# Kernel optimization log

Hardware: AMD Instinct MI355X
Metric: run time of the kernel (lower is better)

Reference implementation:

```python
import jax, jax.numpy as jnp
import numpy as np
from jax import lax

N, T, H, E = 50000, 200, 128, 1600000


def setup_inputs() -> dict:
    key = jax.random.key(0)
    ks = jax.random.split(key, 32)
    s = 0.05
    inp = {}
    inp["lightcurve"] = jax.random.normal(ks[0], (N, T), dtype=jnp.float32)
    inp["edge_index"] = jax.random.randint(ks[1], (2, E), 0, N, dtype=jnp.int32)
    # LSTM layer 0 (input_dim=1) and layer 1 (input H), PyTorch gate order i,f,g,o
    inp["W_ih0"] = jax.random.normal(ks[2], (4 * H, 1), jnp.float32) * s
    inp["W_hh0"] = jax.random.normal(ks[3], (4 * H, H), jnp.float32) * s
    inp["b_ih0"] = jnp.zeros((4 * H,), jnp.float32)
    inp["b_hh0"] = jnp.zeros((4 * H,), jnp.float32)
    inp["W_ih1"] = jax.random.normal(ks[4], (4 * H, H), jnp.float32) * s
    inp["W_hh1"] = jax.random.normal(ks[5], (4 * H, H), jnp.float32) * s
    inp["b_ih1"] = jnp.zeros((4 * H,), jnp.float32)
    inp["b_hh1"] = jnp.zeros((4 * H,), jnp.float32)
    # 3 GCN conv layers + LayerNorms
    for i in range(3):
        inp[f"Wg{i}"] = jax.random.normal(ks[6 + i], (H, H), jnp.float32) * s
        inp[f"bg{i}"] = jnp.zeros((H,), jnp.float32)
        inp[f"gamma{i}"] = jnp.ones((H,), jnp.float32)
        inp[f"beta{i}"] = jnp.zeros((H,), jnp.float32)
    inp["W_out"] = jax.random.normal(ks[10], (H, 1), jnp.float32) * s
    inp["b_out"] = jnp.zeros((1,), jnp.float32)
    return inp


def _lstm_encode(x, W_ih0, W_hh0, b_ih0, b_hh0, W_ih1, W_hh1, b_ih1, b_hh1):
    # x: [N, T, 1] -> final hidden of layer 2: [N, H]. Both layers fused in one scan.
    n = x.shape[0]
    h = W_hh0.shape[1]

    def cell(xt, hs, cs, Wih, Whh, bih, bhh):
        g = xt @ Wih.T + hs @ Whh.T + (bih + bhh)
        i, f, gg, o = jnp.split(g, 4, axis=-1)
        cs = jax.nn.sigmoid(f) * cs + jax.nn.sigmoid(i) * jnp.tanh(gg)
        hs = jax.nn.sigmoid(o) * jnp.tanh(cs)
        return hs, cs

    def step(carry, x_t):
        h1, c1, h2, c2 = carry
        h1, c1 = cell(x_t, h1, c1, W_ih0, W_hh0, b_ih0, b_hh0)
        h2, c2 = cell(h1, h2, c2, W_ih1, W_hh1, b_ih1, b_hh1)
        return (h1, c1, h2, c2), None

    z = jnp.zeros((n, h), x.dtype)
    (_, _, h2, _), _ = lax.scan(step, (z, z, z, z), jnp.swapaxes(x, 0, 1))
    return h2


def _forward(lightcurve, W_ih0, W_hh0, b_ih0, b_hh0, W_ih1, W_hh1, b_ih1, b_hh1,
             Wg0, bg0, gamma0, beta0, Wg1, bg1, gamma1, beta1, Wg2, bg2, gamma2, beta2,
             W_out, b_out, edge_index):
    n = lightcurve.shape[0]
    h = _lstm_encode(lightcurve[..., None], W_ih0, W_hh0, b_ih0, b_hh0,
                     W_ih1, W_hh1, b_ih1, b_hh1)
    # GCN normalization (PyG GCNConv defaults: add self-loops, symmetric norm)
    loops = jnp.arange(n, dtype=edge_index.dtype)
    row = jnp.concatenate([edge_index[0], loops])  # source
    col = jnp.concatenate([edge_index[1], loops])  # target
    deg = jax.ops.segment_sum(jnp.ones_like(col, dtype=h.dtype), col, num_segments=n)
    dinv = lax.rsqrt(jnp.maximum(deg, 1.0))
    enorm = dinv[row] * dinv[col]  # [E+N]
    for Wg, bg, gm, bt in ((Wg0, bg0, gamma0, beta0), (Wg1, bg1, gamma1, beta1), (Wg2, bg2, gamma2, beta2)):
        h_prev = h
        msg = (h @ Wg)[row] * enorm[:, None]            # gather + scale
        h = jax.ops.segment_sum(msg, col, num_segments=n) + bg  # scatter-add
        mu = h.mean(-1, keepdims=True)                  # LayerNorm
        var = jnp.mean((h - mu) ** 2, axis=-1, keepdims=True)
        h = (h - mu) * lax.rsqrt(var + 1e-5) * gm + bt
        h = jax.nn.relu(h)
        h = h + h_prev  # dropout is identity in eval mode
    pooled = h.mean(axis=0, keepdims=True)  # [1, H]
    return pooled @ W_out + b_out           # [1, 1]


def reference(lightcurve, edge_index, W_ih0, W_hh0, b_ih0, b_hh0,
              W_ih1, W_hh1, b_ih1, b_hh1,
              Wg0, bg0, gamma0, beta0, Wg1, bg1, gamma1, beta1,
              Wg2, bg2, gamma2, beta2, W_out, b_out):
    return _forward(lightcurve, W_ih0, W_hh0, b_ih0, b_hh0, W_ih1, W_hh1, b_ih1, b_hh1,
                    Wg0, bg0, gamma0, beta0, Wg1, bg1, gamma1, beta1,
                    Wg2, bg2, gamma2, beta2, W_out, b_out, edge_index)
```

## Files before the change

kernel.cpp:

```cpp
#include <hip/hip_runtime.h>

#define NN 50000
#define TT 200
#define HH 128
#define EE 1600000

typedef _Float16 f16x8 __attribute__((ext_vector_type(8)));
typedef float f32x4 __attribute__((ext_vector_type(4)));

__device__ __forceinline__ float sigf(float x) {
    return __builtin_amdgcn_rcpf(1.f + __expf(-x));
}
__device__ __forceinline__ float tanhf_(float x) {
    return 1.f - 2.f * __builtin_amdgcn_rcpf(__expf(2.f * x) + 1.f);
}
__device__ __forceinline__ f32x4 sig4(f32x4 x) {
    f32x4 r; r[0] = sigf(x[0]); r[1] = sigf(x[1]); r[2] = sigf(x[2]); r[3] = sigf(x[3]); return r;
}
__device__ __forceinline__ f32x4 tanh4(f32x4 x) {
    f32x4 r; r[0] = tanhf_(x[0]); r[1] = tanhf_(x[1]); r[2] = tanhf_(x[2]); r[3] = tanhf_(x[3]); return r;
}
__device__ __forceinline__ f32x4 splat4(float s) { f32x4 r = {s, s, s, s}; return r; }
__device__ __forceinline__ unsigned short f2h_bits(float x) {
    _Float16 h = (_Float16)x;
    union { _Float16 h; unsigned short u; } cv; cv.h = h; return cv.u;
}
__device__ __forceinline__ float h2f_bits(unsigned short u) {
    union { _Float16 h; unsigned short u; } cv; cv.u = u; return (float)cv.h;
}

__global__ void pack_w(const float* __restrict__ W, unsigned short* __restrict__ out) {
    int tile = blockIdx.x;
    int jn = tile >> 2, kk = tile & 3;
    int L = threadIdx.x;
    int n = jn * 16 + (L & 15);
    int k0 = kk * 32 + (L >> 4) * 8;
    unsigned short* dst = out + (size_t)tile * 512 + L * 8;
#pragma unroll
    for (int i = 0; i < 8; ++i) dst[i] = f2h_bits(W[n * 128 + k0 + i]);
}

__global__ void bias_prep(const float* __restrict__ bih0, const float* __restrict__ bhh0,
                          const float* __restrict__ bih1, const float* __restrict__ bhh1,
                          const float* __restrict__ wih0,
                          float* __restrict__ b0g, float* __restrict__ b1g, float* __restrict__ wxg) {
    int i = blockIdx.x * 256 + threadIdx.x;
    if (i < 512) {
        b0g[i] = bih0[i] + bhh0[i];
        b1g[i] = bih1[i] + bhh1[i];
        wxg[i] = wih0[i];
    }
}

__global__ void transpose_lc(const float* __restrict__ lc, float* __restrict__ xT) {
    __shared__ float tile[32][33];
    int tx = threadIdx.x, ty = threadIdx.y;
    int n0 = blockIdx.y * 32, t0 = blockIdx.x * 32;
#pragma unroll
    for (int i = 0; i < 32; i += 8) {
        int n = n0 + ty + i, t = t0 + tx;
        if (n < NN && t < TT) tile[ty + i][tx] = lc[(size_t)n * TT + t];
    }
    __syncthreads();
#pragma unroll
    for (int i = 0; i < 32; i += 8) {
        int t = t0 + ty + i, n = n0 + tx;
        if (n < NN && t < TT) xT[(size_t)t * NN + n] = tile[tx][ty + i];
    }
}


#define MFMA16(A, B, C) __builtin_amdgcn_mfma_f32_16x16x32_f16((A), (B), (C), 0, 0, 0)

#define MMC(HB, PI, PF, PG, PO, KK) {                                          \
    f16x8 bI_ = *reinterpret_cast<const f16x8*>((PI) + (KK) * 512);            \
    f16x8 bF_ = *reinterpret_cast<const f16x8*>((PF) + (KK) * 512);            \
    f16x8 bG_ = *reinterpret_cast<const f16x8*>((PG) + (KK) * 512);            \
    f16x8 bO_ = *reinterpret_cast<const f16x8*>((PO) + (KK) * 512);            \
    f16x8 a0_ = *reinterpret_cast<const f16x8*>(&(HB)[col][(KK) * 32 + quad * 8]);      \
    f16x8 a1_ = *reinterpret_cast<const f16x8*>(&(HB)[16 + col][(KK) * 32 + quad * 8]); \
    aI0 = MFMA16(a0_, bI_, aI0); aI1 = MFMA16(a1_, bI_, aI1);                  \
    aF0 = MFMA16(a0_, bF_, aF0); aF1 = MFMA16(a1_, bF_, aF1);                  \
    aG0 = MFMA16(a0_, bG_, aG0); aG1 = MFMA16(a1_, bG_, aG1);                  \
    aO0 = MFMA16(a0_, bO_, aO0); aO1 = MFMA16(a1_, bO_, aO1);                  \
}

#define ACT0N(RT, C, H, AI, AF, AG, AO) {                                      \
    f32x4 xv_ = *reinterpret_cast<const f32x4*>(&xs[(RT) * 16 + quad * 4]);    \
    f32x4 gi_ = AI + splat4(bI) + xv_ * splat4(wI);                            \
    f32x4 gf_ = AF + splat4(bF) + xv_ * splat4(wF);                            \
    f32x4 gg_ = AG + splat4(bG) + xv_ * splat4(wG);                            \
    f32x4 go_ = AO + splat4(bO) + xv_ * splat4(wO);                            \
    C = sig4(gf_) * C + sig4(gi_) * tanh4(gg_);                                \
    H = sig4(go_) * tanh4(C);                                                  \
}

#define ACT1N(C, H, AI, AF, AG, AO) {                                          \
    f32x4 gi_ = AI + splat4(bI);                                               \
    f32x4 gf_ = AF + splat4(bF);                                               \
    f32x4 gg_ = AG + splat4(bG);                                               \
    f32x4 go_ = AO + splat4(bO);                                               \
    C = sig4(gf_) * C + sig4(gi_) * tanh4(gg_);                                \
    H = sig4(go_) * tanh4(C);                                                  \
}

#define WRH(HB, RT, H)                                                         \
    (HB)[(RT) * 16 + quad * 4 + 0][j_] = f2h_bits((H)[0]);                     \
    (HB)[(RT) * 16 + quad * 4 + 1][j_] = f2h_bits((H)[1]);                     \
    (HB)[(RT) * 16 + quad * 4 + 2][j_] = f2h_bits((H)[2]);                     \
    (HB)[(RT) * 16 + quad * 4 + 3][j_] = f2h_bits((H)[3]);

#define STEP(PB, RB, T)                                                        \
    {                      \
        f32x4 aI0 = {}, aI1 = {}, aF0 = {}, aF1 = {};                          \
        f32x4 aG0 = {}, aG1 = {}, aO0 = {}, aO1 = {};                          \
        MMC(h1s[RB], p0I, p0F, p0G, p0O, 0)                                    \
        MMC(h1s[RB], p0I, p0F, p0G, p0O, 1)                                    \
        MMC(h1s[RB], p0I, p0F, p0G, p0O, 2)                                    \
        MMC(h1s[RB], p0I, p0F, p0G, p0O, 3)                                    \
        const float bI = b0s[j_], bF = b0s[128 + j_];                          \
        const float bG = b0s[256 + j_], bO = b0s[384 + j_];                    \
        const float wI = wxs[j_], wF = wxs[128 + j_];                          \
        const float wG = wxs[256 + j_], wO = wxs[384 + j_];                    \
        f32x4 h1v0, h1v1;                                                      \
        ACT0N(0, c1_0, h1v0, aI0, aF0, aG0, aO0)                               \
        ACT0N(1, c1_1, h1v1, aI1, aF1, aG1, aO1)                               \
        WRH(h1s[PB], 0, h1v0)                                                  \
        WRH(h1s[PB], 1, h1v1)                                                  \
    }                                                                          \
    __syncthreads();                                                           \
    {             \
        f32x4 aI0 = {}, aI1 = {}, aF0 = {}, aF1 = {};                          \
        f32x4 aG0 = {}, aG1 = {}, aO0 = {}, aO1 = {};                          \
        MMC(h1s[PB], u0I, u0F, u0G, u0O, 0)                                    \
        MMC(h1s[PB], u0I, u0F, u0G, u0O, 1)                                    \
        MMC(h1s[PB], u0I, u0F, u0G, u0O, 2)                                    \
        MMC(h1s[PB], u0I, u0F, u0G, u0O, 3)                                    \
        MMC(h2s[RB], v0I, v0F, v0G, v0O, 0)                                    \
        MMC(h2s[RB], v0I, v0F, v0G, v0O, 1)                                    \
        MMC(h2s[RB], v0I, v0F, v0G, v0O, 2)                                    \
        MMC(h2s[RB], v0I, v0F, v0G, v0O, 3)                                    \
        const float bI = b1s[j_], bF = b1s[128 + j_];                          \
        const float bG = b1s[256 + j_], bO = b1s[384 + j_];                    \
        f32x4 h2v0, h2v1;                                                      \
        ACT1N(c2_0, h2v0, aI0, aF0, aG0, aO0)                                  \
        ACT1N(c2_1, h2v1, aI1, aF1, aG1, aO1)                                  \
        WRH(h2s[PB], 0, h2v0)                                                  \
        WRH(h2s[PB], 1, h2v1)                                                  \
        if (tid < 32) {                                                        \
            int n_ = n0 + tid;                                                 \
            xs[tid] = ((T) + 1 < TT && n_ < NN)                                \
                          ? xT[(size_t)((T) + 1) * NN + n_] : 0.f;             \
        }                                                                      \
    }                                                                          \
    __syncthreads();

__global__ __launch_bounds__(512, 2) void lstm_kernel(
    const float* __restrict__ xT,
    const unsigned short* __restrict__ w0p,
    const unsigned short* __restrict__ w1ip,
    const unsigned short* __restrict__ w1hp,
    const float* __restrict__ b0g, const float* __restrict__ b1g,
    const float* __restrict__ wxg,
    float* __restrict__ h2out) {
    __shared__ unsigned short h1s[2][32][136];
    __shared__ unsigned short h2s[2][32][136];
    __shared__ __align__(16) float xs[32];
    __shared__ float b0s[512], b1s[512], wxs[512];

    const int tid = threadIdx.x;
    const int w = tid >> 6;
    const int lane = tid & 63;
    const int col = lane & 15;
    const int quad = lane >> 4;
    const int n0 = blockIdx.x * 32;
    const int j_ = w * 16 + col;

    for (int i = tid; i < 2 * 32 * 136; i += 512) {
        (&h1s[0][0][0])[i] = 0; (&h2s[0][0][0])[i] = 0;
    }
    if (tid < 512) { b0s[tid] = b0g[tid]; b1s[tid] = b1g[tid]; wxs[tid] = wxg[tid]; }
    if (tid < 32) { int n = n0 + tid; xs[tid] = (n < NN) ? xT[n] : 0.f; }

    const unsigned short* p0I = w0p + (size_t)w * 2048 + lane * 8;
    const unsigned short* p0F = w0p + (size_t)(8 + w) * 2048 + lane * 8;
    const unsigned short* p0G = w0p + (size_t)(16 + w) * 2048 + lane * 8;
    const unsigned short* p0O = w0p + (size_t)(24 + w) * 2048 + lane * 8;
    const unsigned short* u0I = w1ip + (size_t)w * 2048 + lane * 8;
    const unsigned short* u0F = w1ip + (size_t)(8 + w) * 2048 + lane * 8;
    const unsigned short* u0G = w1ip + (size_t)(16 + w) * 2048 + lane * 8;
    const unsigned short* u0O = w1ip + (size_t)(24 + w) * 2048 + lane * 8;
    const unsigned short* v0I = w1hp + (size_t)w * 2048 + lane * 8;
    const unsigned short* v0F = w1hp + (size_t)(8 + w) * 2048 + lane * 8;
    const unsigned short* v0G = w1hp + (size_t)(16 + w) * 2048 + lane * 8;
    const unsigned short* v0O = w1hp + (size_t)(24 + w) * 2048 + lane * 8;

    f32x4 c1_0 = {}, c1_1 = {}, c2_0 = {}, c2_1 = {};

    __syncthreads();

#pragma unroll 1
    for (int tt = 0; tt < TT; tt += 2) {
        STEP(0, 1, tt)
        STEP(1, 0, tt + 1)
    }

    for (int i = tid; i < 32 * 128; i += 512) {
        int m = i >> 7, j = i & 127;
        int n = n0 + m;
        if (n < NN) h2out[(size_t)n * HH + j] = h2f_bits(h2s[1][m][j]);
    }
}

__global__ void deg_init(float* __restrict__ deg) {
    int i = blockIdx.x * 256 + threadIdx.x;
    if (i < NN) deg[i] = 1.f;
}
__global__ void deg_edges(const int* __restrict__ ei, float* __restrict__ deg) {
    int e = blockIdx.x * 256 + threadIdx.x;
    if (e < EE) unsafeAtomicAdd(&deg[ei[EE + e]], 1.f);
}
__global__ void dinv_k(const float* __restrict__ deg, float* __restrict__ dinv) {
    int i = blockIdx.x * 256 + threadIdx.x;
    if (i < NN) dinv[i] = rsqrtf(fmaxf(deg[i], 1.f));
}

__global__ void scan_off(const float* __restrict__ deg, int* __restrict__ off) {
    __shared__ int sp[256];
    const int tid = threadIdx.x;
    const int chunk = (NN + 255) / 256;
    const int i0 = tid * chunk;
    int s = 0;
    for (int i = 0; i < chunk; ++i) {
        int idx = i0 + i;
        if (idx < NN) s += (int)deg[idx] - 1;
    }
    sp[tid] = s;
    __syncthreads();
    for (int o = 1; o < 256; o <<= 1) {
        int v = (tid >= o) ? sp[tid - o] : 0;
        __syncthreads();
        sp[tid] += v;
        __syncthreads();
    }
    int run = sp[tid] - s;
    for (int i = 0; i < chunk; ++i) {
        int idx = i0 + i;
        if (idx < NN) { off[idx] = run; run += (int)deg[idx] - 1; }
    }
    if (tid == 255) off[NN] = sp[255];
}

__global__ void csr_fill(const int* __restrict__ ei, const float* __restrict__ dinv,
                         const int* __restrict__ off, int* __restrict__ cur,
                         int* __restrict__ crow, float* __restrict__ cw) {
    int e = blockIdx.x * 256 + threadIdx.x;
    if (e >= EE) return;
    int r = ei[e], c = ei[EE + e];
    int p = atomicAdd(&cur[c], 1);
    int idx = off[c] + p;
    crow[idx] = r;
    cw[idx] = dinv[r] * dinv[c];
}

__global__ void gcn_gemm(const float* __restrict__ h, const float* __restrict__ Wg,
                         float* __restrict__ hw) {
    __shared__ float hsT[128][36];
    int tid = threadIdx.x;
    int n0 = blockIdx.x * 32;
#pragma unroll
    for (int c = 0; c < 16; ++c) {
        int lin = c * 256 + tid;
        int m = lin >> 7, k = lin & 127;
        int n = n0 + m;
        hsT[k][m] = (n < NN) ? h[(size_t)n * HH + k] : 0.f;
    }
    __syncthreads();
    int j = tid & 127, p = tid >> 7;
    float acc[16];
#pragma unroll
    for (int m = 0; m < 16; ++m) acc[m] = 0.f;
    for (int k = 0; k < 128; ++k) {
        float wg = Wg[k * 128 + j];
        const float4* hp = reinterpret_cast<const float4*>(&hsT[k][p * 16]);
        float4 a = hp[0], b = hp[1], c = hp[2], d = hp[3];
        acc[0]  += a.x * wg; acc[1]  += a.y * wg; acc[2]  += a.z * wg; acc[3]  += a.w * wg;
        acc[4]  += b.x * wg; acc[5]  += b.y * wg; acc[6]  += b.z * wg; acc[7]  += b.w * wg;
        acc[8]  += c.x * wg; acc[9]  += c.y * wg; acc[10] += c.z * wg; acc[11] += c.w * wg;
        acc[12] += d.x * wg; acc[13] += d.y * wg; acc[14] += d.z * wg; acc[15] += d.w * wg;
    }
#pragma unroll
    for (int m = 0; m < 16; ++m) {
        int n = n0 + p * 16 + m;
        if (n < NN) hw[(size_t)n * HH + j] = acc[m];
    }
}

__global__ __launch_bounds__(256) void gcn_agg(
    const float* __restrict__ hw, const int* __restrict__ off,
    const int* __restrict__ crow, const float* __restrict__ cw,
    const float* __restrict__ dinv, const float* __restrict__ bg,
    const float* __restrict__ gamma, const float* __restrict__ beta,
    float* __restrict__ h) {
    __shared__ float xch[4][2];
    const int tid = threadIdx.x;
    const int half = tid >> 7;
    const int f = tid & 127;
    const int v = blockIdx.x * 2 + half;
    const float d = dinv[v];
    float acc = bg[f] + d * d * hw[v * HH + f];
    const int s1 = off[v + 1];
    for (int s = off[v]; s < s1; ++s) {
        int r = crow[s];
        float wv = cw[s];
        acc = fmaf(wv, hw[r * HH + f], acc);
    }
    float sum = acc, sq = acc * acc;
#pragma unroll
    for (int o = 32; o; o >>= 1) { sum += __shfl_xor(sum, o); sq += __shfl_xor(sq, o); }
    int wid = tid >> 6;
    if ((tid & 63) == 0) { xch[wid][0] = sum; xch[wid][1] = sq; }
    __syncthreads();
    sum += xch[wid ^ 1][0]; sq += xch[wid ^ 1][1];
    float mu = sum * (1.f / 128.f);
    float var = sq * (1.f / 128.f) - mu * mu;
    float rn = rsqrtf(var + 1e-5f);
    float o = (acc - mu) * rn * gamma[f] + beta[f];
    h[v * HH + f] = fmaxf(o, 0.f) + h[v * HH + f];
}

__global__ void pool_k(const float* __restrict__ h, float* __restrict__ pooled) {
    int j = threadIdx.x & 127, p = threadIdx.x >> 7;
    float s = 0.f;
    for (int n = blockIdx.x * 2 + p; n < NN; n += 512) s += h[(size_t)n * HH + j];
    unsafeAtomicAdd(&pooled[j], s);
}

__global__ void final_k(const float* __restrict__ pooled, const float* __restrict__ Wout,
                        const float* __restrict__ bout, float* __restrict__ out) {
    int lane = threadIdx.x;
    float s = pooled[lane] * Wout[lane] + pooled[lane + 64] * Wout[lane + 64];
#pragma unroll
    for (int o = 32; o; o >>= 1) s += __shfl_xor(s, o);
    if (lane == 0) out[0] = s * (1.f / (float)NN) + bout[0];
}

extern "C" void kernel_launch(void* const* d_in, const int* in_sizes, int n_in,
                              void* d_out, int out_size, void* d_ws, size_t ws_size,
                              hipStream_t stream) {
    const float* lc   = (const float*)d_in[0];
    const int*   ei   = (const int*)d_in[1];
    const float* Wih0 = (const float*)d_in[2];
    const float* Whh0 = (const float*)d_in[3];
    const float* bih0 = (const float*)d_in[4];
    const float* bhh0 = (const float*)d_in[5];
    const float* Wih1 = (const float*)d_in[6];
    const float* Whh1 = (const float*)d_in[7];
    const float* bih1 = (const float*)d_in[8];
    const float* bhh1 = (const float*)d_in[9];
    const float* Wout = (const float*)d_in[22];
    const float* bout = (const float*)d_in[23];
    float* out = (float*)d_out;

    float* ws   = (float*)d_ws;
    float* h    = ws;
    float* hw   = ws + 6400000;
    float* xT   = ws + 6400000;
    int*   off  = (int*)(ws + 12800000);
    int*   cur  = off + 50048;
    int*   crow = cur + 50048;
    float* cw   = (float*)(crow + EE);
    float* P      = ws + 16400064;
    float* deg    = P;
    float* dinv   = deg + 50000;
    float* b0g    = dinv + 50000;
    float* b1g    = b0g + 512;
    float* wxg    = b1g + 512;
    float* pooled = wxg + 512;
    unsigned short* w0p  = (unsigned short*)(pooled + 128);
    unsigned short* w1ip = w0p + 65536;
    unsigned short* w1hp = w1ip + 65536;

    pack_w<<<128, 64, 0, stream>>>(Whh0, w0p);
    pack_w<<<128, 64, 0, stream>>>(Wih1, w1ip);
    pack_w<<<128, 64, 0, stream>>>(Whh1, w1hp);
    bias_prep<<<2, 256, 0, stream>>>(bih0, bhh0, bih1, bhh1, Wih0, b0g, b1g, wxg);
    {
        dim3 g((TT + 31) / 32, (NN + 31) / 32), b(32, 8);
        transpose_lc<<<g, b, 0, stream>>>(lc, xT);
    }
    deg_init<<<(NN + 255) / 256, 256, 0, stream>>>(deg);
    deg_edges<<<(EE + 255) / 256, 256, 0, stream>>>(ei, deg);
    dinv_k<<<(NN + 255) / 256, 256, 0, stream>>>(deg, dinv);

    lstm_kernel<<<(NN + 31) / 32, 512, 0, stream>>>(xT, w0p, w1ip, w1hp, b0g, b1g, wxg, h);

    hipMemsetAsync(cur, 0, 50000 * sizeof(int), stream);
    scan_off<<<1, 256, 0, stream>>>(deg, off);
    csr_fill<<<(EE + 255) / 256, 256, 0, stream>>>(ei, dinv, off, cur, crow, cw);

    for (int l = 0; l < 3; ++l) {
        const float* Wg = (const float*)d_in[10 + 4 * l];
        const float* bg = (const float*)d_in[11 + 4 * l];
        const float* gm = (const float*)d_in[12 + 4 * l];
        const float* bt = (const float*)d_in[13 + 4 * l];
        gcn_gemm<<<(NN + 31) / 32, 256, 0, stream>>>(h, Wg, hw);
        gcn_agg<<<NN / 2, 256, 0, stream>>>(hw, off, crow, cw, dinv, bg, gm, bt, h);
    }

    hipMemsetAsync(pooled, 0, HH * sizeof(float), stream);
    pool_k<<<256, 256, 0, stream>>>(h, pooled);
    final_k<<<1, 64, 0, stream>>>(pooled, Wout, bout, out);
}
```

Baseline: 7.872 ms.

## Skew LSTM layers across timesteps to use one barrier per step

```diff
diff --git a/kernel.cpp b/kernel.cpp
--- a/kernel.cpp
+++ b/kernel.cpp
@@ -6,6 +6,8 @@
 #define EE 1600000
 
 typedef _Float16 f16x8 __attribute__((ext_vector_type(8)));
+typedef _Float16 f16x4 __attribute__((ext_vector_type(4)));
+typedef __fp16 fp16x2 __attribute__((ext_vector_type(2)));
 typedef float f32x4 __attribute__((ext_vector_type(4)));
 
 __device__ __forceinline__ float sigf(float x) {
@@ -21,23 +23,22 @@
     f32x4 r; r[0] = tanhf_(x[0]); r[1] = tanhf_(x[1]); r[2] = tanhf_(x[2]); r[3] = tanhf_(x[3]); return r;
 }
 __device__ __forceinline__ f32x4 splat4(float s) { f32x4 r = {s, s, s, s}; return r; }
-__device__ __forceinline__ unsigned short f2h_bits(float x) {
-    _Float16 h = (_Float16)x;
-    union { _Float16 h; unsigned short u; } cv; cv.h = h; return cv.u;
-}
-__device__ __forceinline__ float h2f_bits(unsigned short u) {
-    union { _Float16 h; unsigned short u; } cv; cv.u = u; return (float)cv.h;
-}
-
-__global__ void pack_w(const float* __restrict__ W, unsigned short* __restrict__ out) {
+__device__ __forceinline__ f16x4 pack4(f32x4 v) {
+    struct P { fp16x2 lo, hi; } p;
+    p.lo = __builtin_amdgcn_cvt_pkrtz(v[0], v[1]);
+    p.hi = __builtin_amdgcn_cvt_pkrtz(v[2], v[3]);
+    return __builtin_bit_cast(f16x4, p);
+}
+
+__global__ void pack_w(const float* __restrict__ W, _Float16* __restrict__ out) {
     int tile = blockIdx.x;
     int jn = tile >> 2, kk = tile & 3;
     int L = threadIdx.x;
     int n = jn * 16 + (L & 15);
     int k0 = kk * 32 + (L >> 4) * 8;
-    unsigned short* dst = out + (size_t)tile * 512 + L * 8;
-#pragma unroll
-    for (int i = 0; i < 8; ++i) dst[i] = f2h_bits(W[n * 128 + k0 + i]);
+    _Float16* dst = out + (size_t)tile * 512 + L * 8;
+#pragma unroll
+    for (int i = 0; i < 8; ++i) dst[i] = (_Float16)W[n * 128 + k0 + i];
 }
 
 __global__ void bias_prep(const float* __restrict__ bih0, const float* __restrict__ bhh0,
@@ -72,143 +73,149 @@
 
 #define MFMA16(A, B, C) __builtin_amdgcn_mfma_f32_16x16x32_f16((A), (B), (C), 0, 0, 0)
 
-#define MMC(HB, PI, PF, PG, PO, KK) {                                          \
-    f16x8 bI_ = *reinterpret_cast<const f16x8*>((PI) + (KK) * 512);            \
-    f16x8 bF_ = *reinterpret_cast<const f16x8*>((PF) + (KK) * 512);            \
-    f16x8 bG_ = *reinterpret_cast<const f16x8*>((PG) + (KK) * 512);            \
-    f16x8 bO_ = *reinterpret_cast<const f16x8*>((PO) + (KK) * 512);            \
-    f16x8 a0_ = *reinterpret_cast<const f16x8*>(&(HB)[col][(KK) * 32 + quad * 8]);      \
-    f16x8 a1_ = *reinterpret_cast<const f16x8*>(&(HB)[16 + col][(KK) * 32 + quad * 8]); \
-    aI0 = MFMA16(a0_, bI_, aI0); aI1 = MFMA16(a1_, bI_, aI1);                  \
-    aF0 = MFMA16(a0_, bF_, aF0); aF1 = MFMA16(a1_, bF_, aF1);                  \
-    aG0 = MFMA16(a0_, bG_, aG0); aG1 = MFMA16(a1_, bG_, aG1);                  \
-    aO0 = MFMA16(a0_, bO_, aO0); aO1 = MFMA16(a1_, bO_, aO1);                  \
-}
-
-#define ACT0N(RT, C, H, AI, AF, AG, AO) {                                      \
-    f32x4 xv_ = *reinterpret_cast<const f32x4*>(&xs[(RT) * 16 + quad * 4]);    \
-    f32x4 gi_ = AI + splat4(bI) + xv_ * splat4(wI);                            \
-    f32x4 gf_ = AF + splat4(bF) + xv_ * splat4(wF);                            \
-    f32x4 gg_ = AG + splat4(bG) + xv_ * splat4(wG);                            \
-    f32x4 go_ = AO + splat4(bO) + xv_ * splat4(wO);                            \
-    C = sig4(gf_) * C + sig4(gi_) * tanh4(gg_);                                \
-    H = sig4(go_) * tanh4(C);                                                  \
-}
-
-#define ACT1N(C, H, AI, AF, AG, AO) {                                          \
-    f32x4 gi_ = AI + splat4(bI);                                               \
-    f32x4 gf_ = AF + splat4(bF);                                               \
-    f32x4 gg_ = AG + splat4(bG);                                               \
-    f32x4 go_ = AO + splat4(bO);                                               \
-    C = sig4(gf_) * C + sig4(gi_) * tanh4(gg_);                                \
-    H = sig4(go_) * tanh4(C);                                                  \
-}
-
-#define WRH(HB, RT, H)                                                         \
-    (HB)[(RT) * 16 + quad * 4 + 0][j_] = f2h_bits((H)[0]);                     \
-    (HB)[(RT) * 16 + quad * 4 + 1][j_] = f2h_bits((H)[1]);                     \
-    (HB)[(RT) * 16 + quad * 4 + 2][j_] = f2h_bits((H)[2]);                     \
-    (HB)[(RT) * 16 + quad * 4 + 3][j_] = f2h_bits((H)[3]);
-
-#define STEP(PB, RB, T)                                                        \
-    {                      \
-        f32x4 aI0 = {}, aI1 = {}, aF0 = {}, aF1 = {};                          \
-        f32x4 aG0 = {}, aG1 = {}, aO0 = {}, aO1 = {};                          \
-        MMC(h1s[RB], p0I, p0F, p0G, p0O, 0)                                    \
-        MMC(h1s[RB], p0I, p0F, p0G, p0O, 1)                                    \
-        MMC(h1s[RB], p0I, p0F, p0G, p0O, 2)                                    \
-        MMC(h1s[RB], p0I, p0F, p0G, p0O, 3)                                    \
-        const float bI = b0s[j_], bF = b0s[128 + j_];                          \
-        const float bG = b0s[256 + j_], bO = b0s[384 + j_];                    \
-        const float wI = wxs[j_], wF = wxs[128 + j_];                          \
-        const float wG = wxs[256 + j_], wO = wxs[384 + j_];                    \
-        f32x4 h1v0, h1v1;                                                      \
-        ACT0N(0, c1_0, h1v0, aI0, aF0, aG0, aO0)                               \
-        ACT0N(1, c1_1, h1v1, aI1, aF1, aG1, aO1)                               \
-        WRH(h1s[PB], 0, h1v0)                                                  \
-        WRH(h1s[PB], 1, h1v1)                                                  \
-    }                                                                          \
-    __syncthreads();                                                           \
-    {             \
-        f32x4 aI0 = {}, aI1 = {}, aF0 = {}, aF1 = {};                          \
-        f32x4 aG0 = {}, aG1 = {}, aO0 = {}, aO1 = {};                          \
-        MMC(h1s[PB], u0I, u0F, u0G, u0O, 0)                                    \
-        MMC(h1s[PB], u0I, u0F, u0G, u0O, 1)                                    \
-        MMC(h1s[PB], u0I, u0F, u0G, u0O, 2)                                    \
-        MMC(h1s[PB], u0I, u0F, u0G, u0O, 3)                                    \
-        MMC(h2s[RB], v0I, v0F, v0G, v0O, 0)                                    \
-        MMC(h2s[RB], v0I, v0F, v0G, v0O, 1)                                    \
-        MMC(h2s[RB], v0I, v0F, v0G, v0O, 2)                                    \
-        MMC(h2s[RB], v0I, v0F, v0G, v0O, 3)                                    \
-        const float bI = b1s[j_], bF = b1s[128 + j_];                          \
-        const float bG = b1s[256 + j_], bO = b1s[384 + j_];                    \
-        f32x4 h2v0, h2v1;                                                      \
-        ACT1N(c2_0, h2v0, aI0, aF0, aG0, aO0)                                  \
-        ACT1N(c2_1, h2v1, aI1, aF1, aG1, aO1)                                  \
-        WRH(h2s[PB], 0, h2v0)                                                  \
-        WRH(h2s[PB], 1, h2v1)                                                  \
-        if (tid < 32) {                                                        \
-            int n_ = n0 + tid;                                                 \
-            xs[tid] = ((T) + 1 < TT && n_ < NN)                                \
-                          ? xT[(size_t)((T) + 1) * NN + n_] : 0.f;             \
-        }                                                                      \
-    }                                                                          \
-    __syncthreads();
+#define MMCW(WB, HR, KK) {                                                      \
+    const _Float16* wb_ = (WB) + (size_t)(KK) * 512 + lane * 8;                 \
+    f16x8 wI_ = *reinterpret_cast<const f16x8*>(wb_ + (size_t)(0 * 8 + wj) * 2048); \
+    f16x8 wF_ = *reinterpret_cast<const f16x8*>(wb_ + (size_t)(1 * 8 + wj) * 2048); \
+    f16x8 wG_ = *reinterpret_cast<const f16x8*>(wb_ + (size_t)(2 * 8 + wj) * 2048); \
+    f16x8 wO_ = *reinterpret_cast<const f16x8*>(wb_ + (size_t)(3 * 8 + wj) * 2048); \
+    f16x8 h0_ = *reinterpret_cast<const f16x8*>(&(HR)[col][(KK) * 32 + quad * 8]);      \
+    f16x8 h1_ = *reinterpret_cast<const f16x8*>(&(HR)[16 + col][(KK) * 32 + quad * 8]); \
+    aI0 = MFMA16(wI_, h0_, aI0); aI1 = MFMA16(wI_, h1_, aI1);                   \
+    aF0 = MFMA16(wF_, h0_, aF0); aF1 = MFMA16(wF_, h1_, aF1);                   \
+    aG0 = MFMA16(wG_, h0_, aG0); aG1 = MFMA16(wG_, h1_, aG1);                   \
+    aO0 = MFMA16(wO_, h0_, aO0); aO1 = MFMA16(wO_, h1_, aO1);                   \
+}
+
+#define EPIL0(NT, C, HV, AI, AF, AG, AO, XB) {                                  \
+    f32x4 bI_ = *reinterpret_cast<const f32x4*>(&b0s[j0]);                      \
+    f32x4 bF_ = *reinterpret_cast<const f32x4*>(&b0s[128 + j0]);                \
+    f32x4 bG_ = *reinterpret_cast<const f32x4*>(&b0s[256 + j0]);                \
+    f32x4 bO_ = *reinterpret_cast<const f32x4*>(&b0s[384 + j0]);                \
+    f32x4 wIv_ = *reinterpret_cast<const f32x4*>(&wxs[j0]);                     \
+    f32x4 wFv_ = *reinterpret_cast<const f32x4*>(&wxs[128 + j0]);               \
+    f32x4 wGv_ = *reinterpret_cast<const f32x4*>(&wxs[256 + j0]);               \
+    f32x4 wOv_ = *reinterpret_cast<const f32x4*>(&wxs[384 + j0]);               \
+    f32x4 xv_ = splat4(xs[XB][(NT) * 16 + col]);                                \
+    f32x4 gi_ = AI + bI_ + xv_ * wIv_;                                          \
+    f32x4 gf_ = AF + bF_ + xv_ * wFv_;                                          \
+    f32x4 gg_ = AG + bG_ + xv_ * wGv_;                                          \
+    f32x4 go_ = AO + bO_ + xv_ * wOv_;                                          \
+    C = sig4(gf_) * C + sig4(gi_) * tanh4(gg_);                                 \
+    HV = sig4(go_) * tanh4(C);                                                  \
+}
+
+#define EPIL1(NT, C, HV, AI, AF, AG, AO) {                                      \
+    f32x4 bI_ = *reinterpret_cast<const f32x4*>(&b1s[j0]);                      \
+    f32x4 bF_ = *reinterpret_cast<const f32x4*>(&b1s[128 + j0]);                \
+    f32x4 bG_ = *reinterpret_cast<const f32x4*>(&b1s[256 + j0]);                \
+    f32x4 bO_ = *reinterpret_cast<const f32x4*>(&b1s[384 + j0]);                \
+    f32x4 gi_ = AI + bI_;                                                       \
+    f32x4 gf_ = AF + bF_;                                                       \
+    f32x4 gg_ = AG + bG_;                                                       \
+    f32x4 go_ = AO + bO_;                                                       \
+    C = sig4(gf_) * C + sig4(gi_) * tanh4(gg_);                                 \
+    HV = sig4(go_) * tanh4(C);                                                  \
+}
+
+#define WRHV(DST, NT, HV) \
+    *reinterpret_cast<f16x4*>(&(DST)[(NT) * 16 + col][j0]) = pack4(HV);
 
 __global__ __launch_bounds__(512, 2) void lstm_kernel(
     const float* __restrict__ xT,
-    const unsigned short* __restrict__ w0p,
-    const unsigned short* __restrict__ w1ip,
-    const unsigned short* __restrict__ w1hp,
+    const _Float16* __restrict__ w0p,
+    const _Float16* __restrict__ w1ip,
+    const _Float16* __restrict__ w1hp,
     const float* __restrict__ b0g, const float* __restrict__ b1g,
     const float* __restrict__ wxg,
     float* __restrict__ h2out) {
-    __shared__ unsigned short h1s[2][32][136];
-    __shared__ unsigned short h2s[2][32][136];
-    __shared__ __align__(16) float xs[32];
-    __shared__ float b0s[512], b1s[512], wxs[512];
+    __shared__ _Float16 h1s[2][32][136];
+    __shared__ _Float16 h2s[2][32][136];
+    __shared__ __align__(16) float xs[2][32];
+    __shared__ __align__(16) float b0s[512], b1s[512], wxs[512];
 
     const int tid = threadIdx.x;
     const int w = tid >> 6;
+    const int wj = __builtin_amdgcn_readfirstlane(w);
     const int lane = tid & 63;
     const int col = lane & 15;
     const int quad = lane >> 4;
     const int n0 = blockIdx.x * 32;
-    const int j_ = w * 16 + col;
-
-    for (int i = tid; i < 2 * 32 * 136; i += 512) {
-        (&h1s[0][0][0])[i] = 0; (&h2s[0][0][0])[i] = 0;
-    }
+    const int j0 = wj * 16 + quad * 4;
+
+    for (int i = tid; i < 32 * 136; i += 512) (&h2s[1][0][0])[i] = (_Float16)0;
     if (tid < 512) { b0s[tid] = b0g[tid]; b1s[tid] = b1g[tid]; wxs[tid] = wxg[tid]; }
-    if (tid < 32) { int n = n0 + tid; xs[tid] = (n < NN) ? xT[n] : 0.f; }
-
-    const unsigned short* p0I = w0p + (size_t)w * 2048 + lane * 8;
-    const unsigned short* p0F = w0p + (size_t)(8 + w) * 2048 + lane * 8;
-    const unsigned short* p0G = w0p + (size_t)(16 + w) * 2048 + lane * 8;
-    const unsigned short* p0O = w0p + (size_t)(24 + w) * 2048 + lane * 8;
-    const unsigned short* u0I = w1ip + (size_t)w * 2048 + lane * 8;
-    const unsigned short* u0F = w1ip + (size_t)(8 + w) * 2048 + lane * 8;
-    const unsigned short* u0G = w1ip + (size_t)(16 + w) * 2048 + lane * 8;
-    const unsigned short* u0O = w1ip + (size_t)(24 + w) * 2048 + lane * 8;
-    const unsigned short* v0I = w1hp + (size_t)w * 2048 + lane * 8;
-    const unsigned short* v0F = w1hp + (size_t)(8 + w) * 2048 + lane * 8;
-    const unsigned short* v0G = w1hp + (size_t)(16 + w) * 2048 + lane * 8;
-    const unsigned short* v0O = w1hp + (size_t)(24 + w) * 2048 + lane * 8;
+    if (tid < 32) {
+        int n = n0 + tid;
+        xs[0][tid] = (n < NN) ? xT[n] : 0.f;
+        xs[1][tid] = (n < NN) ? xT[(size_t)NN + n] : 0.f;
+    }
 
     f32x4 c1_0 = {}, c1_1 = {}, c2_0 = {}, c2_1 = {};
 
     __syncthreads();
 
+    {
+        f32x4 z = {};
+        f32x4 h1v0, h1v1;
+        EPIL0(0, c1_0, h1v0, z, z, z, z, 0)
+        EPIL0(1, c1_1, h1v1, z, z, z, z, 0)
+        WRHV(h1s[1], 0, h1v0)
+        WRHV(h1s[1], 1, h1v1)
+    }
+    __syncthreads();
+
 #pragma unroll 1
-    for (int tt = 0; tt < TT; tt += 2) {
-        STEP(0, 1, tt)
-        STEP(1, 0, tt + 1)
-    }
-
-    for (int i = tid; i < 32 * 128; i += 512) {
-        int m = i >> 7, j = i & 127;
-        int n = n0 + m;
-        if (n < NN) h2out[(size_t)n * HH + j] = h2f_bits(h2s[1][m][j]);
+    for (int k = 0; k < TT - 1; ++k) {
+        const int wp = k & 1;
+        const int rp = wp ^ 1;
+        _Float16 (*h1r)[136] = h1s[rp];
+        _Float16 (*h2r)[136] = h2s[rp];
+        _Float16 (*h1w)[136] = h1s[wp];
+        _Float16 (*h2w)[136] = h2s[wp];
+        {
+            f32x4 aI0 = {}, aI1 = {}, aF0 = {}, aF1 = {};
+            f32x4 aG0 = {}, aG1 = {}, aO0 = {}, aO1 = {};
+            MMCW(w1ip, h1r, 0) MMCW(w1ip, h1r, 1) MMCW(w1ip, h1r, 2) MMCW(w1ip, h1r, 3)
+            MMCW(w1hp, h2r, 0) MMCW(w1hp, h2r, 1) MMCW(w1hp, h2r, 2) MMCW(w1hp, h2r, 3)
+            f32x4 h2v0, h2v1;
+            EPIL1(0, c2_0, h2v0, aI0, aF0, aG0, aO0)
+            EPIL1(1, c2_1, h2v1, aI1, aF1, aG1, aO1)
+            WRHV(h2w, 0, h2v0)
+            WRHV(h2w, 1, h2v1)
+        }
+        if (tid < 32) {
+            int n_ = n0 + tid;
+            float xv = 0.f;
+            if (k + 2 < TT && n_ < NN) xv = xT[(size_t)(k + 2) * NN + n_];
+            xs[wp][tid] = xv;
+        }
+        {
+            f32x4 aI0 = {}, aI1 = {}, aF0 = {}, aF1 = {};
+            f32x4 aG0 = {}, aG1 = {}, aO0 = {}, aO1 = {};
+            MMCW(w0p, h1r, 0) MMCW(w0p, h1r, 1) MMCW(w0p, h1r, 2) MMCW(w0p, h1r, 3)
+            f32x4 h1v0, h1v1;
+            EPIL0(0, c1_0, h1v0, aI0, aF0, aG0, aO0, rp)
+            EPIL0(1, c1_1, h1v1, aI1, aF1, aG1, aO1, rp)
+            WRHV(h1w, 0, h1v0)
+            WRHV(h1w, 1, h1v1)
+        }
+        __syncthreads();
+    }
+
+    {
+        _Float16 (*h1r)[136] = h1s[0];
+        _Float16 (*h2r)[136] = h2s[0];
+        f32x4 aI0 = {}, aI1 = {}, aF0 = {}, aF1 = {};
+        f32x4 aG0 = {}, aG1 = {}, aO0 = {}, aO1 = {};
+        MMCW(w1ip, h1r, 0) MMCW(w1ip, h1r, 1) MMCW(w1ip, h1r, 2) MMCW(w1ip, h1r, 3)
+        MMCW(w1hp, h2r, 0) MMCW(w1hp, h2r, 1) MMCW(w1hp, h2r, 2) MMCW(w1hp, h2r, 3)
+        f32x4 h2v0, h2v1;
+        EPIL1(0, c2_0, h2v0, aI0, aF0, aG0, aO0)
+        EPIL1(1, c2_1, h2v1, aI1, aF1, aG1, aO1)
+        int nA = n0 + col, nB = n0 + 16 + col;
+        if (nA < NN) *reinterpret_cast<f32x4*>(&h2out[(size_t)nA * HH + j0]) = h2v0;
+        if (nB < NN) *reinterpret_cast<f32x4*>(&h2out[(size_t)nB * HH + j0]) = h2v1;
     }
 }
 
@@ -377,9 +384,9 @@
     float* b1g    = b0g + 512;
     float* wxg    = b1g + 512;
     float* pooled = wxg + 512;
-    unsigned short* w0p  = (unsigned short*)(pooled + 128);
-    unsigned short* w1ip = w0p + 65536;
-    unsigned short* w1hp = w1ip + 65536;
+    _Float16* w0p  = (_Float16*)(pooled + 128);
+    _Float16* w1ip = w0p + 65536;
+    _Float16* w1hp = w1ip + 65536;
 
     pack_w<<<128, 64, 0, stream>>>(Whh0, w0p);
     pack_w<<<128, 64, 0, stream>>>(Wih1, w1ip);
```

Result: slower. 9.081 ms (+15.4%).
